# Kernel tuning notes

Measured on AMD Instinct MI355X. Metric: run time of the kernel, lower is better.

Reference implementation:

```python
import jax, jax.numpy as jnp
import numpy as np
import math

EMBED_DIM = 768
NUM_HEADS = 12
HEAD_DIM = EMBED_DIM // NUM_HEADS
R = 16
LORA_ALPHA = 16
SCALING = LORA_ALPHA / math.sqrt(R)  # 4.0
U = 1.0  # ramp_up_steps=0 -> u()=1.0


def lora_linear(x, W, b, A):
    # base F.linear + SingLoRA delta: delta_W = A @ A.T (symmetric)
    base = x @ W.T + b
    delta_W = A @ A.T  # [D, D]
    return base + (x @ delta_W.T) * (U * SCALING)


def setup_inputs() -> dict:
    key = jax.random.key(0)
    ks = jax.random.split(key, 16)
    B, S, D = 2, 2048, EMBED_DIM
    inv = 1.0 / math.sqrt(D)
    d = {
        'query': jax.random.normal(ks[0], (B, S, D), jnp.float32),
        'key': jax.random.normal(ks[1], (B, S, D), jnp.float32),
        'value': jax.random.normal(ks[2], (B, S, D), jnp.float32),
        'Wq': jax.random.normal(ks[3], (D, D), jnp.float32) * inv,
        'bq': jax.random.normal(ks[4], (D,), jnp.float32) * 0.01,
        'Aq': jax.random.normal(ks[5], (D, R), jnp.float32) * 0.01,
        'Wk': jax.random.normal(ks[6], (D, D), jnp.float32) * inv,
        'bk': jax.random.normal(ks[7], (D,), jnp.float32) * 0.01,
        'Ak': jax.random.normal(ks[8], (D, R), jnp.float32) * 0.01,
        'Wv': jax.random.normal(ks[9], (D, D), jnp.float32) * inv,
        'bv': jax.random.normal(ks[10], (D,), jnp.float32) * 0.01,
        'Av': jax.random.normal(ks[11], (D, R), jnp.float32) * 0.01,
        'Wo': jax.random.normal(ks[12], (D, D), jnp.float32) * inv,
        'bo': jax.random.normal(ks[13], (D,), jnp.float32) * 0.01,
    }
    return d


def reference(query, key, value, Wq, bq, Aq, Wk, bk, Ak, Wv, bv, Av, Wo, bo):
    B, S, D = query.shape
    H, hd = NUM_HEADS, HEAD_DIM
    q = lora_linear(query, Wq, bq, Aq)
    k = lora_linear(key, Wk, bk, Ak)
    v = lora_linear(value, Wv, bv, Av)
    # [B, S, D] -> [B, H, S, hd]
    q = q.reshape(B, S, H, hd).transpose(0, 2, 1, 3)
    k = k.reshape(B, S, H, hd).transpose(0, 2, 1, 3)
    v = v.reshape(B, S, H, hd).transpose(0, 2, 1, 3)
    scores = jnp.einsum('bhqd,bhkd->bhqk', q, k) / math.sqrt(hd)
    attn = jax.nn.softmax(scores, axis=-1)
    out = jnp.einsum('bhqk,bhkd->bhqd', attn, v)  # [B, H, S, hd]
    out = out.transpose(0, 2, 1, 3).reshape(B, S, D)
    out = out @ Wo.T + bo
    return out
```

## Files before the change

kernel.cpp:

```cpp
#include <hip/hip_runtime.h>
#include <math.h>
#include <stdint.h>

#define D 768
#define S 2048
#define B_ 2
#define NROWS 4096
#define H 12
#define HD 64
#define R_ 16

typedef _Float16 half_t;
typedef _Float16 half8 __attribute__((ext_vector_type(8)));
typedef _Float16 half4 __attribute__((ext_vector_type(4)));
typedef float floatx4 __attribute__((ext_vector_type(4)));

#define MFMA32(a, b, c) __builtin_amdgcn_mfma_f32_16x16x32_f16(a, b, c, 0, 0, 0)
#define EXP2F(x) __builtin_amdgcn_exp2f(x)

#define SWAIT(N) __builtin_amdgcn_s_waitcnt(0x0F70 | (N))
#define SBAR() __builtin_amdgcn_s_barrier()
#define SETPRIO(N) __builtin_amdgcn_s_setprio(N)

__device__ __forceinline__ void gl_lds16(const void* gp, half_t* lp) {
  __builtin_amdgcn_global_load_lds(
      (const __attribute__((address_space(1))) void*)(gp),
      (__attribute__((address_space(3))) void*)(lp), 16, 0, 0);
}


__global__ __launch_bounds__(256) void prep_kernel(
    const float* __restrict__ q, const float* __restrict__ k,
    const float* __restrict__ v, half_t* __restrict__ xq,
    half_t* __restrict__ xk, half_t* __restrict__ xv,
    const float* __restrict__ Wq, const float* __restrict__ Aq,
    const float* __restrict__ Wk, const float* __restrict__ Ak,
    const float* __restrict__ Wv, const float* __restrict__ Av,
    const float* __restrict__ Wo, half_t* __restrict__ Mq,
    half_t* __restrict__ Mk, half_t* __restrict__ Mv,
    half_t* __restrict__ Mo) {
  const int bid = blockIdx.x;
  if (bid < 9216) {
    const int y = bid / 3072;
    const float* x = (y == 0) ? q : (y == 1) ? k : v;
    half_t* o = (y == 0) ? xq : (y == 1) ? xk : xv;
    int i = (bid - y * 3072) * 1024 + threadIdx.x * 4;
    float4 vv = *reinterpret_cast<const float4*>(x + i);
    half_t tmp[4] = {(half_t)vv.x, (half_t)vv.y, (half_t)vv.z, (half_t)vv.w};
    *reinterpret_cast<uint64_t*>(o + i) = *reinterpret_cast<uint64_t*>(tmp);
  } else {
    const int u = bid - 9216;
    const int y = u / 2304;
    const float* W = (y == 0) ? Wq : (y == 1) ? Wk : (y == 2) ? Wv : Wo;
    const float* A = (y == 0) ? Aq : (y == 1) ? Ak : (y == 2) ? Av : nullptr;
    half_t* M = (y == 0) ? Mq : (y == 1) ? Mk : (y == 2) ? Mv : Mo;
    int idx = (u - y * 2304) * 256 + threadIdx.x;
    int j = idx / D;
    int kk = idx - j * D;
    float acc = W[idx];
    if (A != nullptr) {
      float s = 0.f;
#pragma unroll
      for (int r = 0; r < R_; ++r) s += A[kk * R_ + r] * A[j * R_ + r];
      acc += 4.0f * s;
    }
    M[idx] = (half_t)acc;
  }
}

__global__ __launch_bounds__(256) void gemm_qkv_kernel(
    const half_t* __restrict__ x0, const half_t* __restrict__ x1,
    const half_t* __restrict__ x2, const half_t* __restrict__ m0,
    const half_t* __restrict__ m1, const half_t* __restrict__ m2,
    const float* __restrict__ b0, const float* __restrict__ b1,
    const float* __restrict__ b2, half_t* __restrict__ o0,
    half_t* __restrict__ o1, half_t* __restrict__ o2) {
  constexpr int AG = 8;
  constexpr int G = 16;
  constexpr int PB = G * 512;
  __shared__ __align__(16) half_t smem[3 * PB];

  int lin = blockIdx.x + 6 * (blockIdx.y + 32 * blockIdx.z);
  lin = (lin & 7) * 72 + (lin >> 3);
  const int z = lin / 192;
  const int rem = lin - z * 192;
  const int by = rem / 6;
  const int bx = rem - by * 6;

  const half_t* X = (z == 0) ? x0 : (z == 1) ? x1 : x2;
  const half_t* M = (z == 0) ? m0 : (z == 1) ? m1 : m2;
  const float* bias = (z == 0) ? b0 : (z == 1) ? b1 : b2;
  half_t* Out = (z == 0) ? o0 : (z == 1) ? o1 : o2;

  const int tid = threadIdx.x;
  const int lane = tid & 63;
  const int wv = tid >> 6;
  const int lr = lane & 15;
  const int lq = lane >> 4;
  const int row0 = by * 128;
  const int j0 = bx * 128;
  const int wr = wv >> 1;
  const int wc = wv & 1;

  floatx4 acc[4][4] = {};

#define GSTAGE(soff, k0)                                                      \
  do {                                                                        \
    _Pragma("unroll") for (int gi = 0; gi < 4; ++gi) {                        \
      int g = wv * 4 + gi;                                                    \
      if (g < AG) {                                                           \
        gl_lds16(X + (size_t)(row0 + g * 16 + lr) * D + (k0) + lq * 8,        \
                 smem + (soff) + g * 512);                                    \
      } else {                                                                \
        gl_lds16(M + (size_t)(j0 + (g - AG) * 16 + lr) * D + (k0) + lq * 8,   \
                 smem + (soff) + g * 512);                                    \
      }                                                                       \
    }                                                                         \
  } while (0)

  GSTAGE(0, 0);
  GSTAGE(PB, 32);
  SWAIT(4);
  SBAR();

  int co = 0, so = 2 * PB;
  for (int it = 0; it < D / 32; ++it) {
    if (it + 2 < D / 32) GSTAGE(so, (it + 2) * 32);
    const half_t* Ab = smem + co;
    const half_t* Bb = Ab + AG * 512;
    half8 af[4], bf[4];
#pragma unroll
    for (int t = 0; t < 4; ++t)
      af[t] = *reinterpret_cast<const half8*>(
          &Ab[((wr * 4 + t) * 64 + lane) * 8]);
#pragma unroll
    for (int u = 0; u < 4; ++u)
      bf[u] = *reinterpret_cast<const half8*>(
          &Bb[((wc * 4 + u) * 64 + lane) * 8]);
#pragma unroll
    for (int t = 0; t < 4; ++t)
#pragma unroll
      for (int u = 0; u < 4; ++u) acc[t][u] = MFMA32(af[t], bf[u], acc[t][u]);
    if (it + 2 < D / 32) SWAIT(4); else SWAIT(0);
    SBAR();
    co += PB; if (co == 3 * PB) co = 0;
    so += PB; if (so == 3 * PB) so = 0;
  }
#undef GSTAGE

  float bv[4];
#pragma unroll
  for (int u = 0; u < 4; ++u) bv[u] = bias[j0 + (wc * 4 + u) * 16 + lr];

  if (z == 2) {
    const int bb = row0 >> 11;
    const int kb0 = (row0 & 2047) >> 6;
#pragma unroll
    for (int t = 0; t < 4; ++t) {
#pragma unroll
      for (int u = 0; u < 4; ++u) {
        int gc = j0 + (wc * 4 + u) * 16 + lr;
        int hh = gc >> 6;
        int ud = (gc & 63) >> 4;
        half4 hv;
#pragma unroll
        for (int r = 0; r < 4; ++r) hv[r] = (half_t)(acc[t][u][r] + bv[u]);
        size_t addr = ((size_t)(bb * H + hh) * HD) * S +
                      (size_t)(kb0 + wr) * 4096 +
                      (ud * 2 + ((t >> 1) & 1)) * 512 + lane * 8 + (t & 1) * 4;
        *reinterpret_cast<half4*>(&Out[addr]) = hv;
      }
    }
    return;
  }

#pragma unroll
  for (int t = 0; t < 4; ++t) {
#pragma unroll
    for (int u = 0; u < 4; ++u) {
#pragma unroll
      for (int r = 0; r < 4; ++r) {
        int gr = row0 + (wr * 4 + t) * 16 + lq * 4 + r;
        int gc = j0 + (wc * 4 + u) * 16 + lr;
        Out[(size_t)gr * D + gc] = (half_t)(acc[t][u][r] + bv[u]);
      }
    }
  }
}

__global__ __launch_bounds__(256) void gemm_o_kernel(
    const half_t* __restrict__ Xh, const half_t* __restrict__ M,
    const float* __restrict__ bias, float* __restrict__ Out) {
  constexpr int AG = 8;
  constexpr int G = 16;
  constexpr int PB = G * 512;
  __shared__ __align__(16) half_t smem[3 * PB];

  int lin = blockIdx.x + 12 * blockIdx.y;
  lin = (lin & 7) * 96 + (lin >> 3);
  const int bx = lin % 12;
  const int byy = lin / 12;

  const int tid = threadIdx.x;
  const int lane = tid & 63;
  const int wv = tid >> 6;
  const int lr = lane & 15;
  const int lq = lane >> 4;
  const int row0 = byy * 64;
  const int j0 = bx * 64;
  const int wr = wv >> 1;
  const int wc = wv & 1;

  floatx4 acc[2][2] = {};

#define GSTAGE(soff, k0)                                                       \
  do {                                                                         \
    _Pragma("unroll") for (int gi = 0; gi < 4; ++gi) {                         \
      int g = wv * 4 + gi;                                                     \
      if (g < AG) {                                                            \
        int t = g >> 1, c = g & 1;                                             \
        gl_lds16(                                                              \
            Xh + (size_t)(row0 + t * 16 + lr) * D + (k0) + c * 32 + lq * 8,    \
            smem + (soff) + g * 512);                                          \
      } else {                                                                 \
        int g2 = g - AG;                                                       \
        int u = g2 >> 1, c = g2 & 1;                                           \
        gl_lds16(                                                              \
            M + (size_t)(j0 + u * 16 + lr) * D + (k0) + c * 32 + lq * 8,       \
            smem + (soff) + AG * 512 + g2 * 512);                              \
      }                                                                        \
    }                                                                          \
  } while (0)

  GSTAGE(0, 0);
  GSTAGE(PB, 64);
  SWAIT(4);
  SBAR();

  int co = 0, so = 2 * PB;
  for (int it = 0; it < D / 64; ++it) {
    if (it + 2 < D / 64) GSTAGE(so, (it + 2) * 64);
    const half_t* Ab = smem + co;
    const half_t* Bb = Ab + AG * 512;
#pragma unroll
    for (int c = 0; c < 2; ++c) {
      half8 af[2], bf[2];
#pragma unroll
      for (int t = 0; t < 2; ++t)
        af[t] = *reinterpret_cast<const half8*>(
            &Ab[(((wr * 2 + t) * 2 + c) * 64 + lane) * 8]);
#pragma unroll
      for (int u = 0; u < 2; ++u)
        bf[u] = *reinterpret_cast<const half8*>(
            &Bb[(((wc * 2 + u) * 2 + c) * 64 + lane) * 8]);
#pragma unroll
      for (int t = 0; t < 2; ++t)
#pragma unroll
        for (int u = 0; u < 2; ++u) acc[t][u] = MFMA32(af[t], bf[u], acc[t][u]);
    }
    if (it + 2 < D / 64) SWAIT(4); else SWAIT(0);
    SBAR();
    co += PB; if (co == 3 * PB) co = 0;
    so += PB; if (so == 3 * PB) so = 0;
  }
#undef GSTAGE

  float bv[2];
#pragma unroll
  for (int u = 0; u < 2; ++u) bv[u] = bias[j0 + (wc * 2 + u) * 16 + lr];
#pragma unroll
  for (int t = 0; t < 2; ++t) {
#pragma unroll
    for (int u = 0; u < 2; ++u) {
#pragma unroll
      for (int r = 0; r < 4; ++r) {
        int gr = row0 + (wr * 2 + t) * 16 + lq * 4 + r;
        int gc = j0 + (wc * 2 + u) * 16 + lr;
        Out[(size_t)gr * D + gc] = acc[t][u][r] + bv[u];
      }
    }
  }
}

__global__ __launch_bounds__(256, 3) void attn_mfma_kernel(
    const half_t* __restrict__ Qh, const half_t* __restrict__ Kh,
    const half_t* __restrict__ Vt2, half_t* __restrict__ Oh) {
  __shared__ __align__(16) half_t smem[24576];
  half_t* Ks = smem;
  half_t* Vs = smem + 12288;

  const int tid = threadIdx.x;
  const int lane = tid & 63;
  const int wv = tid >> 6;
  const int qp = wv >> 1;
  const int half_ = wv & 1;
  const int lr = lane & 15;
  const int lq = lane >> 4;

  int lin = blockIdx.x + 32 * (blockIdx.y + 12 * blockIdx.z);
  lin = (lin & 7) * 96 + (lin >> 3);
  const int q0 = (lin & 31) * 64;
  const int hb = lin >> 5;
  const int h = hb % 12;
  const int b = hb / 12;

  const size_t base = (size_t)b * S * D + h * HD;
  const size_t vtbase = (size_t)(b * H + h) * HD * (size_t)S;

  const half_t qscale = (half_t)0.18033688f;
  half8 qf[2][2];
#pragma unroll
  for (int s = 0; s < 2; ++s) {
    const int qw = q0 + (qp * 2 + s) * 16;
#pragma unroll
    for (int c = 0; c < 2; ++c) {
      half8 qv = *reinterpret_cast<const half8*>(
          &Qh[base + (size_t)(qw + lr) * D + c * 32 + lq * 8]);
#pragma unroll
      for (int j = 0; j < 8; ++j) qv[j] = qv[j] * qscale;
      qf[s][c] = qv;
    }
  }

  half8 ones8;
#pragma unroll
  for (int j = 0; j < 8; ++j) ones8[j] = (half_t)1.0f;

  floatx4 o[2][4] = {};
  floatx4 ol[2] = {};

#define STAGE(soff, kb)                                                        \
  do {                                                                         \
    _Pragma("unroll") for (int gi = 0; gi < 4; ++gi) {                         \
      int g = wv * 4 + gi;                                                     \
      if (g < 8) {                                                             \
        int u = g >> 1, c = g & 1;                                             \
        gl_lds16(                                                              \
            Kh + base + (size_t)((kb) + u * 16 + lr) * D + c * 32 + lq * 8,    \
            Ks + (soff) + g * 512);                                            \
      } else {                                                                 \
        int gv = g - 8;                                                        \
        gl_lds16(Vt2 + vtbase + (size_t)(kb)*64 + gv * 512 + lane * 8,         \
                 Vs + (soff) + gv * 512);                                      \
      }                                                                        \
    }                                                                          \
  } while (0)

  STAGE(0, 0);
  STAGE(4096, 64);
  SWAIT(4);
  SBAR();

  int co = 0, so = 8192;
  for (int it = 0; it < S / 64; ++it) {
    if (it + 2 < S / 64) STAGE(so, (it + 2) * 64);

    half8 pv[2];
#pragma unroll
    for (int ui = 0; ui < 2; ++ui) {
      const int u = half_ * 2 + ui;
      half8 kf0 = *reinterpret_cast<const half8*>(
          &Ks[co + ((u * 2 + 0) * 64 + lane) * 8]);
      half8 kf1 = *reinterpret_cast<const half8*>(
          &Ks[co + ((u * 2 + 1) * 64 + lane) * 8]);
      SETPRIO(1);
      floatx4 st0 = {}, st1 = {};
      st0 = MFMA32(kf0, qf[0][0], st0);
      st0 = MFMA32(kf1, qf[0][1], st0);
      st1 = MFMA32(kf0, qf[1][0], st1);
      st1 = MFMA32(kf1, qf[1][1], st1);
      SETPRIO(0);
#pragma unroll
      for (int j = 0; j < 4; ++j) {
        pv[0][4 * ui + j] = (half_t)EXP2F(st0[j]);
        pv[1][4 * ui + j] = (half_t)EXP2F(st1[j]);
      }
    }
    SETPRIO(1);
#pragma unroll
    for (int ud = 0; ud < 4; ++ud) {
      half8 vf8 = *reinterpret_cast<const half8*>(
          &Vs[co + ((ud * 2 + half_) * 64 + lane) * 8]);
      o[0][ud] = MFMA32(pv[0], vf8, o[0][ud]);
      o[1][ud] = MFMA32(pv[1], vf8, o[1][ud]);
    }
    ol[0] = MFMA32(pv[0], ones8, ol[0]);
    ol[1] = MFMA32(pv[1], ones8, ol[1]);
    SETPRIO(0);

    if (it + 2 < S / 64) SWAIT(4); else SWAIT(0);
    SBAR();
    co += 4096; if (co == 12288) co = 0;
    so += 4096; if (so == 12288) so = 0;
  }
#undef STAGE

  float* red = (float*)smem;
  if (half_ == 1) {
#pragma unroll
    for (int s = 0; s < 2; ++s) {
      const int slot = (qp * 2 + s) * 64 + lane;
#pragma unroll
      for (int comp = 0; comp < 16; ++comp)
        red[comp * 260 + slot] = o[s][comp >> 2][comp & 3];
#pragma unroll
      for (int r = 0; r < 4; ++r) red[(16 + r) * 260 + slot] = ol[s][r];
    }
  }
  __syncthreads();
  if (half_ == 0) {
#pragma unroll
    for (int s = 0; s < 2; ++s) {
      const int slot = (qp * 2 + s) * 64 + lane;
      const int qw = q0 + (qp * 2 + s) * 16;
      float linv[4];
#pragma unroll
      for (int r = 0; r < 4; ++r)
        linv[r] = 1.0f / (ol[s][r] + red[(16 + r) * 260 + slot]);
#pragma unroll
      for (int ud = 0; ud < 4; ++ud) {
#pragma unroll
        for (int r = 0; r < 4; ++r) {
          float ov = o[s][ud][r] + red[(ud * 4 + r) * 260 + slot];
          int row = qw + lq * 4 + r;
          int col = h * HD + ud * 16 + lr;
          Oh[(size_t)(b * S + row) * D + col] = (half_t)(ov * linv[r]);
        }
      }
    }
  }
}

extern "C" void kernel_launch(void* const* d_in, const int* in_sizes, int n_in,
                              void* d_out, int out_size, void* d_ws,
                              size_t ws_size, hipStream_t stream) {
  const float* query = (const float*)d_in[0];
  const float* key   = (const float*)d_in[1];
  const float* value = (const float*)d_in[2];
  const float* Wq = (const float*)d_in[3];
  const float* bq = (const float*)d_in[4];
  const float* Aq = (const float*)d_in[5];
  const float* Wk = (const float*)d_in[6];
  const float* bk = (const float*)d_in[7];
  const float* Ak = (const float*)d_in[8];
  const float* Wv = (const float*)d_in[9];
  const float* bv = (const float*)d_in[10];
  const float* Av = (const float*)d_in[11];
  const float* Wo = (const float*)d_in[12];
  const float* bo = (const float*)d_in[13];
  float* out = (float*)d_out;

  half_t* hw = (half_t*)d_ws;
  const size_t XSZ = (size_t)NROWS * D;
  const size_t MSZ = (size_t)D * D;
  half_t* xq = hw;
  half_t* xk = xq + XSZ;
  half_t* xv = xk + XSZ;
  half_t* qh = xv + XSZ;
  half_t* kh = qh + XSZ;
  half_t* vt = kh + XSZ;
  half_t* ab = vt + XSZ;
  half_t* Mq = ab + XSZ;
  half_t* Mk = Mq + MSZ;
  half_t* Mv = Mk + MSZ;
  half_t* Mo = Mv + MSZ;

  prep_kernel<<<18432, 256, 0, stream>>>(query, key, value, xq, xk, xv, Wq, Aq,
                                         Wk, Ak, Wv, Av, Wo, Mq, Mk, Mv, Mo);

  dim3 gq(D / 128, NROWS / 128, 3);
  gemm_qkv_kernel<<<gq, 256, 0, stream>>>(xq, xk, xv, Mq, Mk, Mv, bq, bk, bv,
                                          qh, kh, vt);

  dim3 ga(S / 64, H, B_);
  attn_mfma_kernel<<<ga, 256, 0, stream>>>(qh, kh, vt, ab);

  dim3 go(D / 64, NROWS / 64, 1);
  gemm_o_kernel<<<go, 256, 0, stream>>>(ab, Mo, bo, out);
}
```

Measured before the change: 210.2 us.

## Load K/V fragments directly from global into registers with double buffering

Replaces the LDS triple-buffered K/V staging (global-to-LDS async loads with barriers) in the attention kernel with direct global loads into register fragments, ping-ponged across two register sets. This removes the LDS traffic and per-iteration block barriers and shrinks shared memory to the reduction buffer only, which may allow more resident blocks. In exchange, each wave issues its own uncoalesced-ish global loads without sharing across waves, raising register pressure and relying on L1/L2 for K reuse between waves in the block.

```diff
diff --git a/kernel.cpp b/kernel.cpp
--- a/kernel.cpp
+++ b/kernel.cpp
@@ -285,9 +285,7 @@
 __global__ __launch_bounds__(256, 3) void attn_mfma_kernel(
     const half_t* __restrict__ Qh, const half_t* __restrict__ Kh,
     const half_t* __restrict__ Vt2, half_t* __restrict__ Oh) {
-  __shared__ __align__(16) half_t smem[24576];
-  half_t* Ks = smem;
-  half_t* Vs = smem + 12288;
+  __shared__ float red[20 * 260];
 
   const int tid = threadIdx.x;
   const int lane = tid & 63;
@@ -329,73 +327,60 @@
   floatx4 o[2][4] = {};
   floatx4 ol[2] = {};
 
-#define STAGE(soff, kb)                                                        \
+#define LOADKV(kf, vf, itx)                                                    \
   do {                                                                         \
-    _Pragma("unroll") for (int gi = 0; gi < 4; ++gi) {                         \
-      int g = wv * 4 + gi;                                                     \
-      if (g < 8) {                                                             \
-        int u = g >> 1, c = g & 1;                                             \
-        gl_lds16(                                                              \
-            Kh + base + (size_t)((kb) + u * 16 + lr) * D + c * 32 + lq * 8,    \
-            Ks + (soff) + g * 512);                                            \
-      } else {                                                                 \
-        int gv = g - 8;                                                        \
-        gl_lds16(Vt2 + vtbase + (size_t)(kb)*64 + gv * 512 + lane * 8,         \
-                 Vs + (soff) + gv * 512);                                      \
+    _Pragma("unroll") for (int ui = 0; ui < 2; ++ui)                           \
+        _Pragma("unroll") for (int c = 0; c < 2; ++c)                          \
+            kf[ui * 2 + c] = *reinterpret_cast<const half8*>(                  \
+                &Kh[base +                                                     \
+                    (size_t)((itx)*64 + (half_ * 2 + ui) * 16 + lr) * D +      \
+                    c * 32 + lq * 8]);                                         \
+    _Pragma("unroll") for (int ud = 0; ud < 4; ++ud)                           \
+        vf[ud] = *reinterpret_cast<const half8*>(                              \
+            &Vt2[vtbase + (size_t)(itx)*4096 + (ud * 2 + half_) * 512 +        \
+                 lane * 8]);                                                   \
+  } while (0)
+
+#define COMPUTE(kf, vf)                                                        \
+  do {                                                                         \
+    half8 pv0, pv1;                                                            \
+    _Pragma("unroll") for (int ui = 0; ui < 2; ++ui) {                         \
+      SETPRIO(1);                                                              \
+      floatx4 st0 = {}, st1 = {};                                              \
+      st0 = MFMA32(kf[ui * 2 + 0], qf[0][0], st0);                             \
+      st0 = MFMA32(kf[ui * 2 + 1], qf[0][1], st0);                             \
+      st1 = MFMA32(kf[ui * 2 + 0], qf[1][0], st1);                             \
+      st1 = MFMA32(kf[ui * 2 + 1], qf[1][1], st1);                             \
+      SETPRIO(0);                                                              \
+      _Pragma("unroll") for (int j = 0; j < 4; ++j) {                          \
+        pv0[4 * ui + j] = (half_t)EXP2F(st0[j]);                               \
+        pv1[4 * ui + j] = (half_t)EXP2F(st1[j]);                               \
       }                                                                        \
     }                                                                          \
+    SETPRIO(1);                                                                \
+    _Pragma("unroll") for (int ud = 0; ud < 4; ++ud) {                         \
+      o[0][ud] = MFMA32(pv0, vf[ud], o[0][ud]);                                \
+      o[1][ud] = MFMA32(pv1, vf[ud], o[1][ud]);                                \
+    }                                                                          \
+    ol[0] = MFMA32(pv0, ones8, ol[0]);                                         \
+    ol[1] = MFMA32(pv1, ones8, ol[1]);                                         \
+    SETPRIO(0);                                                                \
   } while (0)
 
-  STAGE(0, 0);
-  STAGE(4096, 64);
-  SWAIT(4);
-  SBAR();
-
-  int co = 0, so = 8192;
-  for (int it = 0; it < S / 64; ++it) {
-    if (it + 2 < S / 64) STAGE(so, (it + 2) * 64);
-
-    half8 pv[2];
-#pragma unroll
-    for (int ui = 0; ui < 2; ++ui) {
-      const int u = half_ * 2 + ui;
-      half8 kf0 = *reinterpret_cast<const half8*>(
-          &Ks[co + ((u * 2 + 0) * 64 + lane) * 8]);
-      half8 kf1 = *reinterpret_cast<const half8*>(
-          &Ks[co + ((u * 2 + 1) * 64 + lane) * 8]);
-      SETPRIO(1);
-      floatx4 st0 = {}, st1 = {};
-      st0 = MFMA32(kf0, qf[0][0], st0);
-      st0 = MFMA32(kf1, qf[0][1], st0);
-      st1 = MFMA32(kf0, qf[1][0], st1);
-      st1 = MFMA32(kf1, qf[1][1], st1);
-      SETPRIO(0);
-#pragma unroll
-      for (int j = 0; j < 4; ++j) {
-        pv[0][4 * ui + j] = (half_t)EXP2F(st0[j]);
-        pv[1][4 * ui + j] = (half_t)EXP2F(st1[j]);
-      }
-    }
-    SETPRIO(1);
-#pragma unroll
-    for (int ud = 0; ud < 4; ++ud) {
-      half8 vf8 = *reinterpret_cast<const half8*>(
-          &Vs[co + ((ud * 2 + half_) * 64 + lane) * 8]);
-      o[0][ud] = MFMA32(pv[0], vf8, o[0][ud]);
-      o[1][ud] = MFMA32(pv[1], vf8, o[1][ud]);
-    }
-    ol[0] = MFMA32(pv[0], ones8, ol[0]);
-    ol[1] = MFMA32(pv[1], ones8, ol[1]);
-    SETPRIO(0);
-
-    if (it + 2 < S / 64) SWAIT(4); else SWAIT(0);
-    SBAR();
-    co += 4096; if (co == 12288) co = 0;
-    so += 4096; if (so == 12288) so = 0;
-  }
-#undef STAGE
-
-  float* red = (float*)smem;
+  half8 kfA[4], vfA[4], kfB[4], vfB[4];
+  LOADKV(kfA, vfA, 0);
+  for (int it = 0; it < 30; it += 2) {
+    LOADKV(kfB, vfB, it + 1);
+    COMPUTE(kfA, vfA);
+    LOADKV(kfA, vfA, it + 2);
+    COMPUTE(kfB, vfB);
+  }
+  LOADKV(kfB, vfB, 31);
+  COMPUTE(kfA, vfA);
+  COMPUTE(kfB, vfB);
+#undef LOADKV
+#undef COMPUTE
+
   if (half_ == 1) {
 #pragma unroll
     for (int s = 0; s < 2; ++s) {
```

Result: slower. 231.8 us (+10.3%).

## Software-pipeline QK^T and exp/PV across iterations in attention loop

Applied to the files above, without the earlier changes.

Restructures the attention inner loop so each iteration issues the QK^T MFMAs and V fragment loads for the next tile before running exp and PV on the previous tile's scores, with ping-pong score and V register buffers. The goal is to overlap transcendental exp work with matrix-core work and hide LDS read latency. This raises register pressure, which may cut occupancy. The V tile is also held in registers across a barrier while its LDS buffer may be reused, so correctness depends on the 3-buffer rotation.

```diff
diff --git a/kernel.cpp b/kernel.cpp
--- a/kernel.cpp
+++ b/kernel.cpp
@@ -346,55 +346,97 @@
     }                                                                          \
   } while (0)
 
+#define QKPHASE(st_, vf_)                                                      \
+  do {                                                                         \
+    _Pragma("unroll") for (int ud = 0; ud < 4; ++ud)                           \
+        vf_[ud] = *reinterpret_cast<const half8*>(                             \
+            &Vs[co + ((ud * 2 + half_) * 64 + lane) * 8]);                     \
+    _Pragma("unroll") for (int ui = 0; ui < 2; ++ui) {                         \
+      const int u = half_ * 2 + ui;                                            \
+      half8 kf0 = *reinterpret_cast<const half8*>(                             \
+          &Ks[co + ((u * 2 + 0) * 64 + lane) * 8]);                            \
+      half8 kf1 = *reinterpret_cast<const half8*>(                             \
+          &Ks[co + ((u * 2 + 1) * 64 + lane) * 8]);                            \
+      SETPRIO(1);                                                              \
+      floatx4 t0 = {}, t1 = {};                                                \
+      t0 = MFMA32(kf0, qf[0][0], t0);                                          \
+      t0 = MFMA32(kf1, qf[0][1], t0);                                          \
+      t1 = MFMA32(kf0, qf[1][0], t1);                                          \
+      t1 = MFMA32(kf1, qf[1][1], t1);                                          \
+      SETPRIO(0);                                                              \
+      st_[0][ui] = t0;                                                         \
+      st_[1][ui] = t1;                                                         \
+    }                                                                          \
+  } while (0)
+
+#define EXPPV(st_, vf_)                                                        \
+  do {                                                                         \
+    half8 pv0, pv1;                                                            \
+    _Pragma("unroll") for (int ui = 0; ui < 2; ++ui)                           \
+        _Pragma("unroll") for (int j = 0; j < 4; ++j) {                        \
+      pv0[4 * ui + j] = (half_t)EXP2F(st_[0][ui][j]);                          \
+      pv1[4 * ui + j] = (half_t)EXP2F(st_[1][ui][j]);                          \
+    }                                                                          \
+    SETPRIO(1);                                                                \
+    _Pragma("unroll") for (int ud = 0; ud < 4; ++ud) {                         \
+      o[0][ud] = MFMA32(pv0, vf_[ud], o[0][ud]);                               \
+      o[1][ud] = MFMA32(pv1, vf_[ud], o[1][ud]);                               \
+    }                                                                          \
+    ol[0] = MFMA32(pv0, ones8, ol[0]);                                         \
+    ol[1] = MFMA32(pv1, ones8, ol[1]);                                         \
+    SETPRIO(0);                                                                \
+  } while (0)
+
+#define ROT()                                                                  \
+  do {                                                                         \
+    co += 4096; if (co == 12288) co = 0;                                       \
+    so += 4096; if (so == 12288) so = 0;                                       \
+  } while (0)
+
   STAGE(0, 0);
   STAGE(4096, 64);
   SWAIT(4);
   SBAR();
 
   int co = 0, so = 8192;
-  for (int it = 0; it < S / 64; ++it) {
-    if (it + 2 < S / 64) STAGE(so, (it + 2) * 64);
-
-    half8 pv[2];
-#pragma unroll
-    for (int ui = 0; ui < 2; ++ui) {
-      const int u = half_ * 2 + ui;
-      half8 kf0 = *reinterpret_cast<const half8*>(
-          &Ks[co + ((u * 2 + 0) * 64 + lane) * 8]);
-      half8 kf1 = *reinterpret_cast<const half8*>(
-          &Ks[co + ((u * 2 + 1) * 64 + lane) * 8]);
-      SETPRIO(1);
-      floatx4 st0 = {}, st1 = {};
-      st0 = MFMA32(kf0, qf[0][0], st0);
-      st0 = MFMA32(kf1, qf[0][1], st0);
-      st1 = MFMA32(kf0, qf[1][0], st1);
-      st1 = MFMA32(kf1, qf[1][1], st1);
-      SETPRIO(0);
-#pragma unroll
-      for (int j = 0; j < 4; ++j) {
-        pv[0][4 * ui + j] = (half_t)EXP2F(st0[j]);
-        pv[1][4 * ui + j] = (half_t)EXP2F(st1[j]);
-      }
-    }
-    SETPRIO(1);
-#pragma unroll
-    for (int ud = 0; ud < 4; ++ud) {
-      half8 vf8 = *reinterpret_cast<const half8*>(
-          &Vs[co + ((ud * 2 + half_) * 64 + lane) * 8]);
-      o[0][ud] = MFMA32(pv[0], vf8, o[0][ud]);
-      o[1][ud] = MFMA32(pv[1], vf8, o[1][ud]);
-    }
-    ol[0] = MFMA32(pv[0], ones8, ol[0]);
-    ol[1] = MFMA32(pv[1], ones8, ol[1]);
-    SETPRIO(0);
-
-    if (it + 2 < S / 64) SWAIT(4); else SWAIT(0);
+  floatx4 stA[2][2], stB[2][2];
+  half8 vfA[4], vfB[4];
+
+  STAGE(so, 2 * 64);
+  QKPHASE(stA, vfA);
+  SWAIT(4);
+  SBAR();
+  ROT();
+
+  for (int it = 1; it < 31; it += 2) {
+    STAGE(so, (it + 2) * 64);
+    QKPHASE(stB, vfB);
+    EXPPV(stA, vfA);
+    SWAIT(4);
     SBAR();
-    co += 4096; if (co == 12288) co = 0;
-    so += 4096; if (so == 12288) so = 0;
-  }
+    ROT();
+    if (it + 3 < 32) {
+      STAGE(so, (it + 3) * 64);
+      QKPHASE(stA, vfA);
+      EXPPV(stB, vfB);
+      SWAIT(4);
+    } else {
+      QKPHASE(stA, vfA);
+      EXPPV(stB, vfB);
+      SWAIT(0);
+    }
+    SBAR();
+    ROT();
+  }
+  QKPHASE(stB, vfB);
+  EXPPV(stA, vfA);
+  EXPPV(stB, vfB);
 #undef STAGE
-
+#undef QKPHASE
+#undef EXPPV
+#undef ROT
+
+  __syncthreads();
   float* red = (float*)smem;
   if (half_ == 1) {
 #pragma unroll
```

Result: slower. 254.9 us (+21.3%).

## Double-buffer attention KV tiles in pairs with one barrier per two tiles

Applied to the files above, without the earlier changes.

Changes the attention inner loop from a 3-slot ring (one 64-key tile per iteration, a barrier every tile) to two 2-tile buffers. Each iteration prefetches the next two tiles and computes two, so there is half as many barriers. LDS grows from 48KB to 64KB and launch bounds drop from 3 to 2 blocks per SM, which reduces occupancy. The full wait (waitcnt 0) before each barrier may also expose more load latency.

```diff
diff --git a/kernel.cpp b/kernel.cpp
--- a/kernel.cpp
+++ b/kernel.cpp
@@ -282,12 +282,12 @@
   }
 }
 
-__global__ __launch_bounds__(256, 3) void attn_mfma_kernel(
+__global__ __launch_bounds__(256, 2) void attn_mfma_kernel(
     const half_t* __restrict__ Qh, const half_t* __restrict__ Kh,
     const half_t* __restrict__ Vt2, half_t* __restrict__ Oh) {
-  __shared__ __align__(16) half_t smem[24576];
+  __shared__ __align__(16) half_t smem[32768];
   half_t* Ks = smem;
-  half_t* Vs = smem + 12288;
+  half_t* Vs = smem + 16384;
 
   const int tid = threadIdx.x;
   const int lane = tid & 63;
@@ -346,54 +346,59 @@
     }                                                                          \
   } while (0)
 
+#define COMP(coff)                                                             \
+  do {                                                                         \
+    half8 pv[2];                                                               \
+    _Pragma("unroll") for (int ui = 0; ui < 2; ++ui) {                         \
+      const int u = half_ * 2 + ui;                                            \
+      half8 kf0 = *reinterpret_cast<const half8*>(                             \
+          &Ks[(coff) + ((u * 2 + 0) * 64 + lane) * 8]);                        \
+      half8 kf1 = *reinterpret_cast<const half8*>(                             \
+          &Ks[(coff) + ((u * 2 + 1) * 64 + lane) * 8]);                        \
+      SETPRIO(1);                                                              \
+      floatx4 st0 = {}, st1 = {};                                              \
+      st0 = MFMA32(kf0, qf[0][0], st0);                                        \
+      st0 = MFMA32(kf1, qf[0][1], st0);                                        \
+      st1 = MFMA32(kf0, qf[1][0], st1);                                        \
+      st1 = MFMA32(kf1, qf[1][1], st1);                                        \
+      SETPRIO(0);                                                              \
+      _Pragma("unroll") for (int j = 0; j < 4; ++j) {                          \
+        pv[0][4 * ui + j] = (half_t)EXP2F(st0[j]);                             \
+        pv[1][4 * ui + j] = (half_t)EXP2F(st1[j]);                             \
+      }                                                                        \
+    }                                                                          \
+    SETPRIO(1);                                                                \
+    _Pragma("unroll") for (int ud = 0; ud < 4; ++ud) {                         \
+      half8 vf8 = *reinterpret_cast<const half8*>(                             \
+          &Vs[(coff) + ((ud * 2 + half_) * 64 + lane) * 8]);                   \
+      o[0][ud] = MFMA32(pv[0], vf8, o[0][ud]);                                 \
+      o[1][ud] = MFMA32(pv[1], vf8, o[1][ud]);                                 \
+    }                                                                          \
+    ol[0] = MFMA32(pv[0], ones8, ol[0]);                                       \
+    ol[1] = MFMA32(pv[1], ones8, ol[1]);                                       \
+    SETPRIO(0);                                                                \
+  } while (0)
+
   STAGE(0, 0);
   STAGE(4096, 64);
-  SWAIT(4);
+  SWAIT(0);
   SBAR();
 
   int co = 0, so = 8192;
-  for (int it = 0; it < S / 64; ++it) {
-    if (it + 2 < S / 64) STAGE(so, (it + 2) * 64);
-
-    half8 pv[2];
-#pragma unroll
-    for (int ui = 0; ui < 2; ++ui) {
-      const int u = half_ * 2 + ui;
-      half8 kf0 = *reinterpret_cast<const half8*>(
-          &Ks[co + ((u * 2 + 0) * 64 + lane) * 8]);
-      half8 kf1 = *reinterpret_cast<const half8*>(
-          &Ks[co + ((u * 2 + 1) * 64 + lane) * 8]);
-      SETPRIO(1);
-      floatx4 st0 = {}, st1 = {};
-      st0 = MFMA32(kf0, qf[0][0], st0);
-      st0 = MFMA32(kf1, qf[0][1], st0);
-      st1 = MFMA32(kf0, qf[1][0], st1);
-      st1 = MFMA32(kf1, qf[1][1], st1);
-      SETPRIO(0);
-#pragma unroll
-      for (int j = 0; j < 4; ++j) {
-        pv[0][4 * ui + j] = (half_t)EXP2F(st0[j]);
-        pv[1][4 * ui + j] = (half_t)EXP2F(st1[j]);
-      }
-    }
-    SETPRIO(1);
-#pragma unroll
-    for (int ud = 0; ud < 4; ++ud) {
-      half8 vf8 = *reinterpret_cast<const half8*>(
-          &Vs[co + ((ud * 2 + half_) * 64 + lane) * 8]);
-      o[0][ud] = MFMA32(pv[0], vf8, o[0][ud]);
-      o[1][ud] = MFMA32(pv[1], vf8, o[1][ud]);
-    }
-    ol[0] = MFMA32(pv[0], ones8, ol[0]);
-    ol[1] = MFMA32(pv[1], ones8, ol[1]);
-    SETPRIO(0);
-
-    if (it + 2 < S / 64) SWAIT(4); else SWAIT(0);
+  for (int it = 0; it < 32; it += 2) {
+    if (it + 2 < 32) {
+      STAGE(so, (it + 2) * 64);
+      STAGE(so + 4096, (it + 3) * 64);
+    }
+    COMP(co);
+    COMP(co + 4096);
+    SWAIT(0);
     SBAR();
-    co += 4096; if (co == 12288) co = 0;
-    so += 4096; if (so == 12288) so = 0;
+    co ^= 8192;
+    so ^= 8192;
   }
 #undef STAGE
+#undef COMP
 
   float* red = (float*)smem;
   if (half_ == 1) {
```

After: 219.6 us. 1.04x slower.
